# Kernel tuning notes

Hardware: AMD Instinct MI355X
Metric: run time of the kernel (lower is better)

Reference implementation:

```python
import jax, jax.numpy as jnp
import numpy as np

B, S, F = 16, 511, 128           # batch, input seq len, n_features
D, H, NB = 512, 8, 6             # embedding_dim, n_heads, n_blocks
DH = D // H                      # d_head
MLP = 4 * D                      # mlp_ratio=4 hard-coded in FxtBlock
OUT = 1                          # out_d
T = S + 1                        # tokens incl. cls
EPS = 1e-5                       # torch LayerNorm default eps


def pos_emb(seq_len, d):
    # matches get_positional_embeddings: sin for even j, cos for odd j (with j-1 exponent)
    i = np.arange(seq_len, dtype=np.float32)[:, None]
    j = np.arange(d)
    je = np.where(j % 2 == 0, j, j - 1).astype(np.float32)
    ang = i / (10000.0 ** (je / d))
    pe = np.where(j % 2 == 0, np.sin(ang), np.cos(ang))
    return jnp.asarray(pe, jnp.float32)


def layernorm(x, g, b):
    m = jnp.mean(x, axis=-1, keepdims=True)
    v = jnp.mean((x - m) ** 2, axis=-1, keepdims=True)
    return (x - m) * jax.lax.rsqrt(v + EPS) * g + b


def setup_inputs() -> dict:
    key = jax.random.key(0)
    ks = jax.random.split(key, 12)
    g = lambda k, shape: jax.random.normal(k, shape, jnp.float32) * 0.02
    return {
        "src": jax.random.normal(ks[0], (B, S, F), jnp.float32),
        "emb_W": g(ks[1], (F, D)), "emb_b": jnp.zeros((D,), jnp.float32),
        "cls_tok": jax.random.uniform(ks[2], (1, D), jnp.float32),
        "ln1_g": jnp.ones((NB, D), jnp.float32), "ln1_b": jnp.zeros((NB, D), jnp.float32),
        "Wq": g(ks[3], (NB, H, DH, DH)), "bq": jnp.zeros((NB, H, DH), jnp.float32),
        "Wk": g(ks[4], (NB, H, DH, DH)), "bk": jnp.zeros((NB, H, DH), jnp.float32),
        "Wv": g(ks[5], (NB, H, DH, DH)), "bv": jnp.zeros((NB, H, DH), jnp.float32),
        "ln2_g": jnp.ones((NB, D), jnp.float32), "ln2_b": jnp.zeros((NB, D), jnp.float32),
        "W1": g(ks[6], (NB, D, MLP)), "b1": jnp.zeros((NB, MLP), jnp.float32),
        "W2": g(ks[7], (NB, MLP, D)), "b2": jnp.zeros((NB, D), jnp.float32),
        "head_W": g(ks[8], (D, OUT)), "head_b": jnp.zeros((OUT,), jnp.float32),
    }


def reference(src, emb_W, emb_b, cls_tok, ln1_g, ln1_b, Wq, bq, Wk, bk, Wv, bv,
              ln2_g, ln2_b, W1, b1, W2, b2, head_W, head_b):
    b = src.shape[0]
    x = src @ emb_W + emb_b                                    # [B,S,D]
    cls = jnp.broadcast_to(cls_tok[None], (b, 1, D))
    x = jnp.concatenate([cls, x], axis=1) + pos_emb(T, D)[None]  # [B,T,D]
    scale = 1.0 / jnp.sqrt(jnp.float32(DH))
    for i in range(NB):
        h = layernorm(x, ln1_g[i], ln1_b[i])
        hh = h.reshape(b, T, H, DH)
        q = jnp.einsum('bthd,hde->bhte', hh, Wq[i]) + bq[i][None, :, None, :]
        k = jnp.einsum('bthd,hde->bhte', hh, Wk[i]) + bk[i][None, :, None, :]
        v = jnp.einsum('bthd,hde->bhte', hh, Wv[i]) + bv[i][None, :, None, :]
        attn = jax.nn.softmax(jnp.einsum('bhse,bhte->bhst', q, k) * scale, axis=-1)
        o = jnp.einsum('bhst,bhte->bhse', attn, v)             # [B,H,T,DH]
        x = x + o.transpose(0, 2, 1, 3).reshape(b, T, D)
        h2 = layernorm(x, ln2_g[i], ln2_b[i])
        x = x + (jax.nn.gelu(h2 @ W1[i] + b1[i], approximate=False) @ W2[i] + b2[i])
    return jax.nn.sigmoid(x[:, 0] @ head_W + head_b)           # [B,OUT]
```

## Files before the change

### kernel.cpp

```cpp
#include <hip/hip_runtime.h>
#include <hip/hip_bf16.h>
#include <math.h>

#define B 16
#define S 511
#define F 128
#define D 512
#define H 8
#define NB 6
#define DH 64
#define MLPD 2048
#define T 512
#define EPS 1e-5f

typedef unsigned short ushort;
typedef __attribute__((ext_vector_type(8))) short short8;
typedef __attribute__((ext_vector_type(4))) float floatx4;

__device__ __forceinline__ ushort f2bf(float f) {
    union { float f; unsigned u; } cv; cv.f = f;
    unsigned r = (cv.u + 0x7fff + ((cv.u >> 16) & 1)) >> 16;
    return (ushort)r;
}

__device__ __forceinline__ float fast_gelu(float x) {
    float z = fabsf(x) * 0.70710678118f;
    float t = 1.0f / (1.0f + 0.3275911f * z);
    float p = ((((1.061405429f * t - 1.453152027f) * t + 1.421413741f) * t
               - 0.284496736f) * t + 0.254829592f) * t;
    float erfv = 1.0f - p * __expf(-z * z);
    erfv = copysignf(erfv, x);
    return 0.5f * x * (1.0f + erfv);
}

__global__ void castsrc_kernel(const float* __restrict__ src, ushort* __restrict__ srcb) {
    int row = blockIdx.x;
    int t = row & (T - 1), b = row >> 9;
    int tid = threadIdx.x;
    ushort v = 0;
    if (t > 0) v = f2bf(src[((size_t)b * S + (t - 1)) * F + tid]);
    srcb[(size_t)row * F + tid] = v;
}

__global__ void wtrans_kernel(const float* __restrict__ W,
                              ushort* __restrict__ Wt,
                              int K, int N) {
    int kb = blockIdx.x * 32, nb = blockIdx.y * 32, mat = blockIdx.z;
    __shared__ float tile[32][33];
    int tid = threadIdx.x;
    int c = tid & 31, r0 = tid >> 5;
    const float* Wm = W + (size_t)mat * K * N;
    ushort* Wtm = Wt + (size_t)mat * K * N;
    #pragma unroll
    for (int l = 0; l < 4; ++l) {
        int r = r0 + l * 8;
        tile[r][c] = Wm[(size_t)(kb + r) * N + nb + c];
    }
    __syncthreads();
    #pragma unroll
    for (int l = 0; l < 4; ++l) {
        int r = r0 + l * 8;
        Wtm[(size_t)(nb + r) * K + kb + c] = f2bf(tile[c][r]);
    }
}

__global__ void wtransq_kernel(const float* __restrict__ Wq, const float* __restrict__ Wk,
                               const float* __restrict__ Wv,
                               ushort* __restrict__ WqT, ushort* __restrict__ WkT,
                               ushort* __restrict__ WvT) {
    int mat = blockIdx.x;
    int which = blockIdx.y;
    const float* W = (which == 0 ? Wq : which == 1 ? Wk : Wv) + (size_t)mat * 4096;
    ushort* O = (which == 0 ? WqT : which == 1 ? WkT : WvT) + (size_t)mat * 4096;
    __shared__ float t[64][65];
    int tid = threadIdx.x;
    int r0 = tid >> 6, c = tid & 63;
    #pragma unroll
    for (int l = 0; l < 16; ++l) {
        int row = r0 * 16 + l;
        t[row][c] = W[row * 64 + c];
    }
    __syncthreads();
    #pragma unroll
    for (int l = 0; l < 16; ++l) {
        int row = r0 * 16 + l;
        O[row * 64 + c] = f2bf(t[c][row]);
    }
}

__device__ __forceinline__ void gload_lds16(const ushort* g, ushort* l) {
    __builtin_amdgcn_global_load_lds((const __attribute__((address_space(1))) unsigned int*)g,
                                     (__attribute__((address_space(3))) unsigned int*)l,
                                     16, 0, 0);
}

#define S_WAITCNT_VM(N) asm volatile("s_waitcnt vmcnt(" #N ")" ::: "memory")

__global__ __launch_bounds__(256) void embed_gemm(const ushort* __restrict__ A,
                                                  const ushort* __restrict__ Bt,
                                                  const float* __restrict__ emb_b,
                                                  const float* __restrict__ cls_tok,
                                                  float* __restrict__ x) {
    __shared__ ushort As[64 * 32];
    __shared__ ushort Bs[64 * 32];
    int tid = threadIdx.x;
    int lane = tid & 63;
    int w = __builtin_amdgcn_readfirstlane(tid >> 6);
    int quad = lane >> 4, l15 = lane & 15;
    int wr = (w >> 1) * 32, wc = (w & 1) * 32;
    int m0 = blockIdx.x * 64, n0 = blockIdx.y * 64;

    floatx4 acc[2][2];
    #pragma unroll
    for (int i = 0; i < 2; ++i)
        #pragma unroll
        for (int j = 0; j < 2; ++j) acc[i][j] = (floatx4)0.f;

    int lrow = lane >> 2;
    int lk = (lane & 3) * 8;
    const ushort* Ag = A + (size_t)(m0 + 16 * w + lrow) * F + lk;
    const ushort* Bg = Bt + (size_t)(n0 + 16 * w + lrow) * F + lk;
    ushort* AsW = &As[16 * w * 32];
    ushort* BsW = &Bs[16 * w * 32];
    int fa = l15 * 32 + quad * 8;

    for (int kt = 0; kt < F; kt += 32) {
        gload_lds16(Ag + kt, AsW);
        gload_lds16(Bg + kt, BsW);
        __syncthreads();
        short8 af[2], bf[2];
        #pragma unroll
        for (int i = 0; i < 2; ++i) af[i] = *(const short8*)&As[(wr + 16 * i) * 32 + fa];
        #pragma unroll
        for (int j = 0; j < 2; ++j) bf[j] = *(const short8*)&Bs[(wc + 16 * j) * 32 + fa];
        #pragma unroll
        for (int i = 0; i < 2; ++i)
            #pragma unroll
            for (int j = 0; j < 2; ++j)
                acc[i][j] = __builtin_amdgcn_mfma_f32_16x16x32_bf16(af[i], bf[j], acc[i][j], 0, 0, 0);
        __syncthreads();
    }

    const float LOG1E4 = 9.210340371976184f;
    int rbase = (lane >> 4) * 4;
    int cidx = lane & 15;
    #pragma unroll
    for (int j = 0; j < 2; ++j) {
        int gc = n0 + wc + 16 * j + cidx;
        float je = (float)(gc & ~1);
        float freq = expf(-(je / (float)D) * LOG1E4);
        float ebv = emb_b[gc];
        float clsv = cls_tok[gc];
        bool odd = (gc & 1);
        #pragma unroll
        for (int i = 0; i < 2; ++i) {
            int gr = m0 + wr + 16 * i + rbase;
            #pragma unroll
            for (int reg = 0; reg < 4; ++reg) {
                int row = gr + reg;
                int t = row & (T - 1);
                float ang = (float)t * freq;
                float pe = odd ? cosf(ang) : sinf(ang);
                float val = (t == 0) ? (clsv + pe) : (acc[i][j][reg] + ebv + pe);
                x[(size_t)row * D + gc] = val;
            }
        }
    }
}

__global__ __launch_bounds__(256) void ln_kernel(const float* __restrict__ xin,
                                                 const float* __restrict__ g,
                                                 const float* __restrict__ bb,
                                                 ushort* __restrict__ out) {
    int lane = threadIdx.x & 63;
    int row = blockIdx.x * 4 + (threadIdx.x >> 6);
    const float* xr = xin + (size_t)row * D + lane * 8;
    float4 a0 = *(const float4*)xr;
    float4 a1 = *(const float4*)(xr + 4);
    float s = a0.x + a0.y + a0.z + a0.w + a1.x + a1.y + a1.z + a1.w;
    #pragma unroll
    for (int off = 1; off < 64; off <<= 1) s += __shfl_xor(s, off);
    float mean = s * (1.0f / (float)D);
    float d0 = a0.x - mean, d1 = a0.y - mean, d2 = a0.z - mean, d3 = a0.w - mean;
    float d4 = a1.x - mean, d5 = a1.y - mean, d6 = a1.z - mean, d7 = a1.w - mean;
    float sq = d0*d0 + d1*d1 + d2*d2 + d3*d3 + d4*d4 + d5*d5 + d6*d6 + d7*d7;
    #pragma unroll
    for (int off = 1; off < 64; off <<= 1) sq += __shfl_xor(sq, off);
    float rstd = rsqrtf(sq * (1.0f / (float)D) + EPS);
    const float* gp = g + lane * 8;
    const float* bp = bb + lane * 8;
    float4 g0 = *(const float4*)gp, g1 = *(const float4*)(gp + 4);
    float4 b0 = *(const float4*)bp, b1 = *(const float4*)(bp + 4);
    short8 o;
    o[0] = (short)f2bf(d0 * rstd * g0.x + b0.x);
    o[1] = (short)f2bf(d1 * rstd * g0.y + b0.y);
    o[2] = (short)f2bf(d2 * rstd * g0.z + b0.z);
    o[3] = (short)f2bf(d3 * rstd * g0.w + b0.w);
    o[4] = (short)f2bf(d4 * rstd * g1.x + b1.x);
    o[5] = (short)f2bf(d5 * rstd * g1.y + b1.y);
    o[6] = (short)f2bf(d6 * rstd * g1.z + b1.z);
    o[7] = (short)f2bf(d7 * rstd * g1.w + b1.w);
    *(short8*)(out + (size_t)row * D + lane * 8) = o;
}

__global__ __launch_bounds__(256) void ln_fuse_kernel(float* __restrict__ x,
                                                      const float* __restrict__ p0,
                                                      const float* __restrict__ g,
                                                      const float* __restrict__ bb,
                                                      ushort* __restrict__ out) {
    int lane = threadIdx.x & 63;
    int row = blockIdx.x * 4 + (threadIdx.x >> 6);
    size_t base = (size_t)row * D + lane * 8;
    float* xr = x + base;
    float4 a0 = *(const float4*)xr;
    float4 a1 = *(const float4*)(xr + 4);
    float4 q0 = *(const float4*)(p0 + base);
    float4 q1 = *(const float4*)(p0 + base + 4);
    a0.x += q0.x; a0.y += q0.y; a0.z += q0.z; a0.w += q0.w;
    a1.x += q1.x; a1.y += q1.y; a1.z += q1.z; a1.w += q1.w;
    *(float4*)xr = a0;
    *(float4*)(xr + 4) = a1;
    float s = a0.x + a0.y + a0.z + a0.w + a1.x + a1.y + a1.z + a1.w;
    #pragma unroll
    for (int off = 1; off < 64; off <<= 1) s += __shfl_xor(s, off);
    float mean = s * (1.0f / (float)D);
    float d0 = a0.x - mean, d1 = a0.y - mean, d2 = a0.z - mean, d3 = a0.w - mean;
    float d4 = a1.x - mean, d5 = a1.y - mean, d6 = a1.z - mean, d7 = a1.w - mean;
    float sq = d0*d0 + d1*d1 + d2*d2 + d3*d3 + d4*d4 + d5*d5 + d6*d6 + d7*d7;
    #pragma unroll
    for (int off = 1; off < 64; off <<= 1) sq += __shfl_xor(sq, off);
    float rstd = rsqrtf(sq * (1.0f / (float)D) + EPS);
    const float* gp = g + lane * 8;
    const float* bp = bb + lane * 8;
    float4 g0 = *(const float4*)gp, g1 = *(const float4*)(gp + 4);
    float4 b0 = *(const float4*)bp, b1 = *(const float4*)(bp + 4);
    short8 o;
    o[0] = (short)f2bf(d0 * rstd * g0.x + b0.x);
    o[1] = (short)f2bf(d1 * rstd * g0.y + b0.y);
    o[2] = (short)f2bf(d2 * rstd * g0.z + b0.z);
    o[3] = (short)f2bf(d3 * rstd * g0.w + b0.w);
    o[4] = (short)f2bf(d4 * rstd * g1.x + b1.x);
    o[5] = (short)f2bf(d5 * rstd * g1.y + b1.y);
    o[6] = (short)f2bf(d6 * rstd * g1.z + b1.z);
    o[7] = (short)f2bf(d7 * rstd * g1.w + b1.w);
    *(short8*)(out + (size_t)row * D + lane * 8) = o;
}

__global__ __launch_bounds__(256) void qkv_kernel(
        const ushort* __restrict__ hb,
        const ushort* __restrict__ WqT, const float* __restrict__ bq,
        const ushort* __restrict__ WkT, const float* __restrict__ bk,
        const ushort* __restrict__ WvT, const float* __restrict__ bv,
        ushort* __restrict__ qo, ushort* __restrict__ ko, ushort* __restrict__ vTo) {
    int m0 = blockIdx.x * 128;
    int hh = blockIdx.y;
    int tid = threadIdx.x;
    int lane = tid & 63;
    int w = __builtin_amdgcn_readfirstlane(tid >> 6);
    int quad = lane >> 4, l15 = lane & 15;

    short8 af[2][2];
    #pragma unroll
    for (int mt = 0; mt < 2; ++mt) {
        const ushort* ab = hb + (size_t)(m0 + w * 32 + mt * 16 + l15) * D + hh * DH + quad * 8;
        af[mt][0] = *(const short8*)(ab);
        af[mt][1] = *(const short8*)(ab + 32);
    }

    floatx4 acc[3][2][4];
    #pragma unroll
    for (int xo = 0; xo < 3; ++xo)
        #pragma unroll
        for (int mt = 0; mt < 2; ++mt)
            #pragma unroll
            for (int nt = 0; nt < 4; ++nt) acc[xo][mt][nt] = (floatx4)0.f;

    #pragma unroll
    for (int xo = 0; xo < 3; ++xo) {
        const ushort* WT = (xo == 0 ? WqT : xo == 1 ? WkT : WvT) + (size_t)hh * 4096;
        #pragma unroll
        for (int nt = 0; nt < 4; ++nt) {
            const ushort* wb = WT + (size_t)(nt * 16 + l15) * 64 + quad * 8;
            short8 bf0 = *(const short8*)(wb);
            short8 bf1 = *(const short8*)(wb + 32);
            #pragma unroll
            for (int mt = 0; mt < 2; ++mt) {
                acc[xo][mt][nt] = __builtin_amdgcn_mfma_f32_16x16x32_bf16(af[mt][0], bf0, acc[xo][mt][nt], 0, 0, 0);
                acc[xo][mt][nt] = __builtin_amdgcn_mfma_f32_16x16x32_bf16(af[mt][1], bf1, acc[xo][mt][nt], 0, 0, 0);
            }
        }
    }

    int bb = m0 >> 9;
    int bh = bb * H + hh;
    #pragma unroll
    for (int mt = 0; mt < 2; ++mt) {
        int trow = m0 + w * 32 + mt * 16 + quad * 4;
        int tt = trow & (T - 1);
        #pragma unroll
        for (int nt = 0; nt < 4; ++nt) {
            int col = nt * 16 + l15;
            float bqv = bq[hh * DH + col];
            float bkv = bk[hh * DH + col];
            float bvv = bv[hh * DH + col];
            #pragma unroll
            for (int reg = 0; reg < 4; ++reg) {
                qo[((size_t)bh * T + tt + reg) * DH + col] = f2bf(acc[0][mt][nt][reg] + bqv);
                ko[((size_t)bh * T + tt + reg) * DH + col] = f2bf(acc[1][mt][nt][reg] + bkv);
                vTo[((size_t)bh * DH + col) * T + tt + reg] = f2bf(acc[2][mt][nt][reg] + bvv);
            }
        }
    }
}

#define PSTRIDE 88
__global__ __launch_bounds__(256) void attn_kernel(const ushort* __restrict__ q,
                                                   const ushort* __restrict__ k,
                                                   const ushort* __restrict__ vT,
                                                   float* __restrict__ x) {
    int bh = blockIdx.x;
    int qt = blockIdx.y;
    int b = bh >> 3, hh = bh & 7;
    int tid = threadIdx.x;
    int lane = tid & 63;
    int w = __builtin_amdgcn_readfirstlane(tid >> 6);
    int quad = lane >> 4, l15 = lane & 15;

    __shared__ __align__(16) ushort smem[22016];
    ushort* Pw = smem + 16384 + w * (16 * PSTRIDE);

    const ushort* qbase = q + ((size_t)bh * T + qt * 64 + w * 16 + l15) * DH + quad * 8;
    short8 Qf0 = *(const short8*)(qbase);
    short8 Qf1 = *(const short8*)(qbase + 32);

    const ushort* kbase = k + (size_t)bh * T * DH;
    const ushort* vbase = vT + (size_t)bh * DH * T;

    int srow = lane >> 2;
    int scol = (lane & 3) * 8;
    const ushort* kg = kbase + (size_t)(w * 16 + srow) * DH + scol;
    const ushort* vg = vbase + (size_t)(w * 16 + srow) * T + scol;
    ushort* ldsK = smem + w * 16 * 32;
    ushort* ldsV = smem + 8192 + w * 16 * 32;

    float l_i[4] = {0.f, 0.f, 0.f, 0.f};
    floatx4 O[4];
    #pragma unroll
    for (int j = 0; j < 4; ++j) O[j] = (floatx4)0.f;

    gload_lds16(kg, ldsK);
    gload_lds16(kg + 32, ldsK + 2048);
    gload_lds16(vg, ldsV);
    gload_lds16(vg + 32, ldsV + 2048);
    __syncthreads();

    for (int kt = 0; kt < T / 64; ++kt) {
        int cur = kt & 1;
        if (kt < T / 64 - 1) {
            int nb = cur ^ 1;
            const ushort* kgn = kg + (size_t)(kt + 1) * 64 * DH;
            const ushort* vgn = vg + (kt + 1) * 64;
            gload_lds16(kgn, ldsK + nb * 4096);
            gload_lds16(kgn + 32, ldsK + nb * 4096 + 2048);
            gload_lds16(vgn, ldsV + nb * 4096);
            gload_lds16(vgn + 32, ldsV + nb * 4096 + 2048);
        }
        const ushort* Kc = smem + cur * 4096;
        const ushort* Vc = smem + 8192 + cur * 4096;

        floatx4 sc[4];
        #pragma unroll
        for (int j = 0; j < 4; ++j) {
            int ro = (j * 16 + l15) * 32 + quad * 8;
            short8 kf0 = *(const short8*)&Kc[ro];
            short8 kf1 = *(const short8*)&Kc[2048 + ro];
            floatx4 s4 = (floatx4)0.f;
            s4 = __builtin_amdgcn_mfma_f32_16x16x32_bf16(Qf0, kf0, s4, 0, 0, 0);
            s4 = __builtin_amdgcn_mfma_f32_16x16x32_bf16(Qf1, kf1, s4, 0, 0, 0);
            sc[j] = s4;
        }
        #pragma unroll
        for (int j = 0; j < 4; ++j) {
            #pragma unroll
            for (int r = 0; r < 4; ++r) {
                float p = __expf(sc[j][r] * 0.125f);
                ushort pb = f2bf(p);
                union { unsigned u; float f; } cv; cv.u = ((unsigned)pb) << 16;
                l_i[r] += cv.f;
                Pw[(quad * 4 + r) * PSTRIDE + j * 16 + l15] = pb;
            }
        }

        short8 af0 = *(const short8*)&Pw[l15 * PSTRIDE + quad * 8];
        short8 af1 = *(const short8*)&Pw[l15 * PSTRIDE + 32 + quad * 8];
        #pragma unroll
        for (int j = 0; j < 4; ++j) {
            int ro = (j * 16 + l15) * 32 + quad * 8;
            short8 vf0 = *(const short8*)&Vc[ro];
            short8 vf1 = *(const short8*)&Vc[2048 + ro];
            O[j] = __builtin_amdgcn_mfma_f32_16x16x32_bf16(af0, vf0, O[j], 0, 0, 0);
            O[j] = __builtin_amdgcn_mfma_f32_16x16x32_bf16(af1, vf1, O[j], 0, 0, 0);
        }
        __syncthreads();
    }

    #pragma unroll
    for (int r = 0; r < 4; ++r) {
        l_i[r] += __shfl_xor(l_i[r], 1);
        l_i[r] += __shfl_xor(l_i[r], 2);
        l_i[r] += __shfl_xor(l_i[r], 4);
        l_i[r] += __shfl_xor(l_i[r], 8);
    }

    float* Ow = (float*)smem + w * 16 * 68;
    #pragma unroll
    for (int r = 0; r < 4; ++r) {
        float rl = 1.0f / l_i[r];
        #pragma unroll
        for (int j = 0; j < 4; ++j)
            Ow[(quad * 4 + r) * 68 + j * 16 + l15] = O[j][r] * rl;
    }
    __syncthreads();
    int r4 = lane >> 4;
    int c16 = lane & 15;
    #pragma unroll
    for (int i = 0; i < 4; ++i) {
        int lrow = i * 4 + r4;
        float4 o = *(const float4*)&Ow[lrow * 68 + c16 * 4];
        int grow = qt * 64 + w * 16 + lrow;
        float* xp = &x[((size_t)(b * T) + grow) * D + hh * DH + c16 * 4];
        float4 xv = *(const float4*)xp;
        xv.x += o.x; xv.y += o.y; xv.z += o.z; xv.w += o.w;
        *(float4*)xp = xv;
    }
}

template<int EPI>
__global__ __launch_bounds__(256, 2) void gemm_db(const ushort* __restrict__ A,
                                                  const ushort* __restrict__ Bt,
                                                  const float* __restrict__ bias,
                                                  void* __restrict__ Cout,
                                                  int N, int K) {
    constexpr int BK = 64;
    __shared__ ushort lds0[256 * BK];
    __shared__ ushort lds1[256 * BK];

    int tid = threadIdx.x;
    int lane = tid & 63;
    int w = __builtin_amdgcn_readfirstlane(tid >> 6);
    int quad = lane >> 4, l15 = lane & 15;
    int wrow = (w >> 1) * 64;
    int wcol = (w & 1) * 64;

    int nwg = gridDim.x;
    int id = blockIdx.x;
    int idx = (id & 7) * (nwg >> 3) + (id >> 3);
    int NTg = N >> 7;
    int mt = idx / NTg;
    int nt = idx - mt * NTg;
    int m0 = mt * 128, n0 = nt * 128;

    int lrow = tid >> 3;
    int lslot = tid & 7;
    int scol = (lslot ^ (lrow & 7)) * 8;
    const ushort* Asrc = A + (size_t)(m0 + lrow) * K + scol;
    const ushort* Bsrc = Bt + (size_t)(n0 + lrow) * K + scol;
    int ldsAoff = (w * 8) * BK;
    int ldsBoff = 128 * BK + (w * 8) * BK;

    int sx0 = ((quad) ^ (l15 & 7)) * 8;
    int sx1 = ((4 + quad) ^ (l15 & 7)) * 8;

    floatx4 acc[4][4];
    #pragma unroll
    for (int i = 0; i < 4; ++i)
        #pragma unroll
        for (int n = 0; n < 4; ++n) acc[i][n] = (floatx4)0.f;

    #define STAGE(t, Lb) do {                                                     \
        const ushort* ap_ = Asrc + (size_t)(t) * BK;                              \
        const ushort* bp_ = Bsrc + (size_t)(t) * BK;                              \
        _Pragma("unroll")                                                         \
        for (int j = 0; j < 4; ++j)                                               \
            gload_lds16(ap_ + (size_t)j * 32 * K, (Lb) + ldsAoff + j * 32 * BK);  \
        _Pragma("unroll")                                                         \
        for (int j = 0; j < 4; ++j)                                               \
            gload_lds16(bp_ + (size_t)j * 32 * K, (Lb) + ldsBoff + j * 32 * BK);  \
    } while (0)

    #define COMP(Lb) do {                                                         \
        const ushort* Ab_ = (Lb);                                                 \
        const ushort* Bb_ = (Lb) + 128 * BK;                                      \
        _Pragma("unroll")                                                         \
        for (int ks = 0; ks < 2; ++ks) {                                          \
            int sx_ = ks ? sx1 : sx0;                                             \
            short8 bfr[4];                                                        \
            _Pragma("unroll")                                                     \
            for (int n = 0; n < 4; ++n)                                           \
                bfr[n] = *(const short8*)&Bb_[(wcol + n * 16 + l15) * BK + sx_];  \
            _Pragma("unroll")                                                     \
            for (int i = 0; i < 4; ++i) {                                         \
                short8 af_ = *(const short8*)&Ab_[(wrow + i * 16 + l15) * BK + sx_]; \
                _Pragma("unroll")                                                 \
                for (int n = 0; n < 4; ++n)                                       \
                    acc[i][n] = __builtin_amdgcn_mfma_f32_16x16x32_bf16(af_, bfr[n], acc[i][n], 0, 0, 0); \
            }                                                                     \
        }                                                                         \
    } while (0)

    int NT = K >> 6;
    STAGE(0, lds0);
    for (int t = 0; t < NT - 2; t += 2) {
        STAGE(t + 1, lds1);
        S_WAITCNT_VM(8);
        __builtin_amdgcn_s_barrier();
        __builtin_amdgcn_s_setprio(1);
        COMP(lds0);
        __builtin_amdgcn_s_setprio(0);
        asm volatile("s_waitcnt lgkmcnt(0)" ::: "memory");
        __builtin_amdgcn_s_barrier();
        STAGE(t + 2, lds0);
        S_WAITCNT_VM(8);
        __builtin_amdgcn_s_barrier();
        __builtin_amdgcn_s_setprio(1);
        COMP(lds1);
        __builtin_amdgcn_s_setprio(0);
        asm volatile("s_waitcnt lgkmcnt(0)" ::: "memory");
        __builtin_amdgcn_s_barrier();
    }
    STAGE(NT - 1, lds1);
    S_WAITCNT_VM(8);
    __builtin_amdgcn_s_barrier();
    __builtin_amdgcn_s_setprio(1);
    COMP(lds0);
    __builtin_amdgcn_s_setprio(0);
    asm volatile("s_waitcnt lgkmcnt(0)" ::: "memory");
    __builtin_amdgcn_s_barrier();
    S_WAITCNT_VM(0);
    __builtin_amdgcn_s_barrier();
    COMP(lds1);

    #undef STAGE
    #undef COMP

    int rbase = quad * 4;
    #pragma unroll
    for (int i = 0; i < 4; ++i) {
        #pragma unroll
        for (int n = 0; n < 4; ++n) {
            int gc = n0 + wcol + n * 16 + l15;
            float bv = bias[gc];
            int gr = m0 + wrow + i * 16 + rbase;
            #pragma unroll
            for (int reg = 0; reg < 4; ++reg) {
                if constexpr (EPI == 0) {
                    ((ushort*)Cout)[(size_t)(gr + reg) * N + gc] =
                        f2bf(fast_gelu(acc[i][n][reg] + bv));
                } else {
                    ((float*)Cout)[(size_t)(gr + reg) * N + gc] = acc[i][n][reg] + bv;
                }
            }
        }
    }
}

__global__ void head_kernel(const float* __restrict__ x,
                            const float* __restrict__ p0,
                            const float* __restrict__ hw,
                            const float* __restrict__ hb,
                            float* __restrict__ out) {
    int b = blockIdx.x;
    int tid = threadIdx.x;
    size_t idx = (size_t)b * T * D + tid;
    float s = (x[idx] + p0[idx]) * hw[tid];
    #pragma unroll
    for (int off = 32; off > 0; off >>= 1) s += __shfl_down(s, off, 64);
    __shared__ float red[8];
    if ((tid & 63) == 0) red[tid >> 6] = s;
    __syncthreads();
    if (tid == 0) {
        float t = 0.f;
        #pragma unroll
        for (int i = 0; i < 8; ++i) t += red[i];
        out[b] = 1.0f / (1.0f + __expf(-(t + hb[0])));
    }
}

extern "C" void kernel_launch(void* const* d_in, const int* in_sizes, int n_in,
                              void* d_out, int out_size, void* d_ws, size_t ws_size,
                              hipStream_t stream) {
    const float* src     = (const float*)d_in[0];
    const float* emb_W   = (const float*)d_in[1];
    const float* emb_b   = (const float*)d_in[2];
    const float* cls_tok = (const float*)d_in[3];
    const float* ln1_g   = (const float*)d_in[4];
    const float* ln1_b   = (const float*)d_in[5];
    const float* Wq      = (const float*)d_in[6];
    const float* bq      = (const float*)d_in[7];
    const float* Wk      = (const float*)d_in[8];
    const float* bk      = (const float*)d_in[9];
    const float* Wv      = (const float*)d_in[10];
    const float* bv      = (const float*)d_in[11];
    const float* ln2_g   = (const float*)d_in[12];
    const float* ln2_b   = (const float*)d_in[13];
    const float* W1      = (const float*)d_in[14];
    const float* b1      = (const float*)d_in[15];
    const float* W2      = (const float*)d_in[16];
    const float* b2      = (const float*)d_in[17];
    const float* head_W  = (const float*)d_in[18];
    const float* head_b  = (const float*)d_in[19];

    const size_t NTOK = (size_t)B * T;
    char* wsb = (char*)d_ws;
    float*  x    = (float*)wsb;      wsb += NTOK * D * 4;
    float*  p0   = (float*)wsb;      wsb += NTOK * D * 4;
    ushort* hbuf = (ushort*)wsb;     wsb += NTOK * D * 2;
    ushort* q    = (ushort*)wsb;     wsb += NTOK * D * 2;
    ushort* k    = (ushort*)wsb;     wsb += NTOK * D * 2;
    ushort* vT   = (ushort*)wsb;     wsb += NTOK * D * 2;
    ushort* u    = (ushort*)wsb;     wsb += NTOK * MLPD * 2;
    ushort* W1t  = (ushort*)wsb;     wsb += (size_t)NB * D * MLPD * 2;
    ushort* W2t  = (ushort*)wsb;     wsb += (size_t)NB * D * MLPD * 2;
    ushort* WqT  = (ushort*)wsb;     wsb += (size_t)NB * H * DH * DH * 2;
    ushort* WkT  = (ushort*)wsb;     wsb += (size_t)NB * H * DH * DH * 2;
    ushort* WvT  = (ushort*)wsb;     wsb += (size_t)NB * H * DH * DH * 2;
    ushort* srcb = (ushort*)wsb;     wsb += NTOK * F * 2;
    ushort* embWt= (ushort*)wsb;     wsb += (size_t)F * D * 2;

    wtrans_kernel<<<dim3(D / 32, MLPD / 32, NB), 256, 0, stream>>>(W1, W1t, D, MLPD);
    wtrans_kernel<<<dim3(MLPD / 32, D / 32, NB), 256, 0, stream>>>(W2, W2t, MLPD, D);
    wtransq_kernel<<<dim3(NB * H, 3), 256, 0, stream>>>(Wq, Wk, Wv, WqT, WkT, WvT);
    wtrans_kernel<<<dim3(F / 32, D / 32, 1), 256, 0, stream>>>(emb_W, embWt, F, D);
    castsrc_kernel<<<B * T, F, 0, stream>>>(src, srcb);

    embed_gemm<<<dim3(B * T / 64, D / 64), 256, 0, stream>>>(srcb, embWt, emb_b, cls_tok, x);

    for (int i = 0; i < NB; ++i) {
        if (i == 0)
            ln_kernel<<<B * T / 4, 256, 0, stream>>>(x, ln1_g, ln1_b, hbuf);
        else
            ln_fuse_kernel<<<B * T / 4, 256, 0, stream>>>(x, p0,
                ln1_g + i * D, ln1_b + i * D, hbuf);
        qkv_kernel<<<dim3(B * T / 128, H), 256, 0, stream>>>(hbuf,
            WqT + (size_t)i * H * DH * DH, bq + (size_t)i * H * DH,
            WkT + (size_t)i * H * DH * DH, bk + (size_t)i * H * DH,
            WvT + (size_t)i * H * DH * DH, bv + (size_t)i * H * DH,
            q, k, vT);
        attn_kernel<<<dim3(B * H, T / 64), 256, 0, stream>>>(q, k, vT, x);
        ln_kernel<<<B * T / 4, 256, 0, stream>>>(x, ln2_g + i * D, ln2_b + i * D, hbuf);
        gemm_db<0><<<dim3((B * T / 128) * (MLPD / 128)), 256, 0, stream>>>(
            hbuf, W1t + (size_t)i * D * MLPD, b1 + (size_t)i * MLPD, u, MLPD, D);
        gemm_db<1><<<dim3((B * T / 128) * (D / 128)), 256, 0, stream>>>(
            u, W2t + (size_t)i * MLPD * D, b2 + (size_t)i * D, p0, D, MLPD);
    }

    head_kernel<<<B, 512, 0, stream>>>(x, p0, head_W, head_b, (float*)d_out);
}
```

Measured before the change: 848.9 us.

## Add 256x256-tile 8-wave GEMM with phased load/MFMA interleave for MLP up-projection

```diff
diff --git a/kernel.cpp b/kernel.cpp
--- a/kernel.cpp
+++ b/kernel.cpp
@@ -95,6 +95,7 @@
 }
 
 #define S_WAITCNT_VM(N) asm volatile("s_waitcnt vmcnt(" #N ")" ::: "memory")
+#define S_WAITCNT_LGKM0 asm volatile("s_waitcnt lgkmcnt(0)" ::: "memory")
 
 __global__ __launch_bounds__(256) void embed_gemm(const ushort* __restrict__ A,
                                                   const ushort* __restrict__ Bt,
@@ -435,11 +436,151 @@
     }
 }
 
-template<int EPI>
+__global__ __launch_bounds__(512, 2) void gemm1_8ph(const ushort* __restrict__ A,
+                                                    const ushort* __restrict__ Bt,
+                                                    const float* __restrict__ bias,
+                                                    ushort* __restrict__ C,
+                                                    int N, int K) {
+    constexpr int BK = 64;
+    constexpr int BUF = 32768;
+    constexpr int BOF = 16384;
+    __shared__ ushort lds[2 * BUF];
+
+    int tid = threadIdx.x;
+    int lane = tid & 63;
+    int w = __builtin_amdgcn_readfirstlane(tid >> 6);
+    int quad = lane >> 4, l15 = lane & 15;
+    int wm = w >> 2, wn = w & 3;
+    int wmr = wm * 128, wnr = wn * 64;
+
+    int nwg = gridDim.x;
+    int id = blockIdx.x;
+    int idx = (id & 7) * (nwg >> 3) + (id >> 3);
+    int NTg = N >> 8;
+    int mt = idx / NTg, nt = idx - mt * NTg;
+    int m0 = mt * 256, n0 = nt * 256;
+
+    int rr = tid >> 3;
+    int scol = ((tid & 7) ^ (rr & 7)) * 8;
+    const ushort* AgS = A + (size_t)(m0 + rr) * K + scol;
+    const ushort* BgS = Bt + (size_t)(n0 + rr) * K + scol;
+    int woff = (w * 8) * BK;
+
+    int sx0 = (quad ^ (l15 & 7)) * 8;
+    int sx1 = ((4 + quad) ^ (l15 & 7)) * 8;
+
+    floatx4 acc[8][4];
+    #pragma unroll
+    for (int i = 0; i < 8; ++i)
+        #pragma unroll
+        for (int n = 0; n < 4; ++n) acc[i][n] = (floatx4)0.f;
+
+    short8 a[4][2], b[4][2];
+
+    #define STG_A(th, h, bb) do {                                                          \
+        gload_lds16(AgS + (size_t)((h) * 128) * K + (size_t)(th) * BK,                     \
+                    (bb) + ((h) * 128) * BK + woff);                                       \
+        gload_lds16(AgS + (size_t)((h) * 128 + 64) * K + (size_t)(th) * BK,                \
+                    (bb) + ((h) * 128 + 64) * BK + woff);                                  \
+    } while (0)
+    #define STG_B(th, h, bb) do {                                                          \
+        gload_lds16(BgS + (size_t)((h) * 128) * K + (size_t)(th) * BK,                     \
+                    (bb) + BOF + ((h) * 128) * BK + woff);                                 \
+        gload_lds16(BgS + (size_t)((h) * 128 + 64) * K + (size_t)(th) * BK,                \
+                    (bb) + BOF + ((h) * 128 + 64) * BK + woff);                            \
+    } while (0)
+
+    #define MFMA_Q(mb, nb2) do {                                                           \
+        _Pragma("unroll")                                                                  \
+        for (int ks = 0; ks < 2; ++ks)                                                     \
+            _Pragma("unroll")                                                              \
+            for (int i = 0; i < 4; ++i)                                                    \
+                _Pragma("unroll")                                                          \
+                for (int n = 0; n < 2; ++n)                                                \
+                    acc[(mb) + i][(nb2) + n] = __builtin_amdgcn_mfma_f32_16x16x32_bf16(    \
+                        a[i][ks], b[(nb2) + n][ks], acc[(mb) + i][(nb2) + n], 0, 0, 0);    \
+    } while (0)
+
+    STG_A(0, 0, lds); STG_A(0, 1, lds); STG_B(0, 0, lds); STG_B(0, 1, lds);
+    STG_A(1, 0, lds + BUF);
+
+    int NT = K >> 6;
+    for (int t = 0; t < NT; ++t) {
+        ushort* bufc = lds + (t & 1) * BUF;
+        ushort* bufn = lds + (((t & 1) ^ 1)) * BUF;
+        bool sn = (t + 1 < NT);
+        if (t == NT - 1) { S_WAITCNT_VM(0); } else { S_WAITCNT_VM(2); }
+        __builtin_amdgcn_s_barrier();
+        #pragma unroll
+        for (int ks = 0; ks < 2; ++ks) {
+            int sx = ks ? sx1 : sx0;
+            #pragma unroll
+            for (int i = 0; i < 4; ++i)
+                a[i][ks] = *(const short8*)&bufc[(wmr + i * 16 + l15) * BK + sx];
+            #pragma unroll
+            for (int n = 0; n < 2; ++n)
+                b[n][ks] = *(const short8*)&bufc[BOF + (wnr + n * 16 + l15) * BK + sx];
+        }
+        if (sn) STG_A(t + 1, 1, bufn);
+        S_WAITCNT_LGKM0;
+        __builtin_amdgcn_s_setprio(1);
+        MFMA_Q(0, 0);
+        __builtin_amdgcn_s_setprio(0);
+        #pragma unroll
+        for (int ks = 0; ks < 2; ++ks) {
+            int sx = ks ? sx1 : sx0;
+            #pragma unroll
+            for (int n = 0; n < 2; ++n)
+                b[2 + n][ks] = *(const short8*)&bufc[BOF + (wnr + (2 + n) * 16 + l15) * BK + sx];
+        }
+        if (sn) STG_B(t + 1, 0, bufn);
+        S_WAITCNT_LGKM0;
+        __builtin_amdgcn_s_setprio(1);
+        MFMA_Q(0, 2);
+        __builtin_amdgcn_s_setprio(0);
+        #pragma unroll
+        for (int ks = 0; ks < 2; ++ks) {
+            int sx = ks ? sx1 : sx0;
+            #pragma unroll
+            for (int i = 0; i < 4; ++i)
+                a[i][ks] = *(const short8*)&bufc[(wmr + (4 + i) * 16 + l15) * BK + sx];
+        }
+        if (sn) STG_B(t + 1, 1, bufn);
+        S_WAITCNT_LGKM0;
+        __builtin_amdgcn_s_setprio(1);
+        MFMA_Q(4, 2);
+        __builtin_amdgcn_s_setprio(0);
+        __builtin_amdgcn_s_barrier();
+        if (t + 2 < NT) STG_A(t + 2, 0, bufc);
+        __builtin_amdgcn_s_setprio(1);
+        MFMA_Q(4, 0);
+        __builtin_amdgcn_s_setprio(0);
+    }
+
+    #undef STG_A
+    #undef STG_B
+    #undef MFMA_Q
+
+    int rbase = quad * 4;
+    #pragma unroll
+    for (int i = 0; i < 8; ++i) {
+        #pragma unroll
+        for (int n = 0; n < 4; ++n) {
+            int gc = n0 + wnr + n * 16 + l15;
+            float bv = bias[gc];
+            int gr = m0 + wmr + i * 16 + rbase;
+            #pragma unroll
+            for (int reg = 0; reg < 4; ++reg) {
+                C[(size_t)(gr + reg) * N + gc] = f2bf(fast_gelu(acc[i][n][reg] + bv));
+            }
+        }
+    }
+}
+
 __global__ __launch_bounds__(256, 2) void gemm_db(const ushort* __restrict__ A,
                                                   const ushort* __restrict__ Bt,
                                                   const float* __restrict__ bias,
-                                                  void* __restrict__ Cout,
+                                                  float* __restrict__ Cout,
                                                   int N, int K) {
     constexpr int BK = 64;
     __shared__ ushort lds0[256 * BK];
@@ -517,7 +658,7 @@
         __builtin_amdgcn_s_setprio(1);
         COMP(lds0);
         __builtin_amdgcn_s_setprio(0);
-        asm volatile("s_waitcnt lgkmcnt(0)" ::: "memory");
+        S_WAITCNT_LGKM0;
         __builtin_amdgcn_s_barrier();
         STAGE(t + 2, lds0);
         S_WAITCNT_VM(8);
@@ -525,7 +666,7 @@
         __builtin_amdgcn_s_setprio(1);
         COMP(lds1);
         __builtin_amdgcn_s_setprio(0);
-        asm volatile("s_waitcnt lgkmcnt(0)" ::: "memory");
+        S_WAITCNT_LGKM0;
         __builtin_amdgcn_s_barrier();
     }
     STAGE(NT - 1, lds1);
@@ -534,7 +675,7 @@
     __builtin_amdgcn_s_setprio(1);
     COMP(lds0);
     __builtin_amdgcn_s_setprio(0);
-    asm volatile("s_waitcnt lgkmcnt(0)" ::: "memory");
+    S_WAITCNT_LGKM0;
     __builtin_amdgcn_s_barrier();
     S_WAITCNT_VM(0);
     __builtin_amdgcn_s_barrier();
@@ -553,12 +694,7 @@
             int gr = m0 + wrow + i * 16 + rbase;
             #pragma unroll
             for (int reg = 0; reg < 4; ++reg) {
-                if constexpr (EPI == 0) {
-                    ((ushort*)Cout)[(size_t)(gr + reg) * N + gc] =
-                        f2bf(fast_gelu(acc[i][n][reg] + bv));
-                } else {
-                    ((float*)Cout)[(size_t)(gr + reg) * N + gc] = acc[i][n][reg] + bv;
-                }
+                Cout[(size_t)(gr + reg) * N + gc] = acc[i][n][reg] + bv;
             }
         }
     }
@@ -648,9 +784,9 @@
             q, k, vT);
         attn_kernel<<<dim3(B * H, T / 64), 256, 0, stream>>>(q, k, vT, x);
         ln_kernel<<<B * T / 4, 256, 0, stream>>>(x, ln2_g + i * D, ln2_b + i * D, hbuf);
-        gemm_db<0><<<dim3((B * T / 128) * (MLPD / 128)), 256, 0, stream>>>(
+        gemm1_8ph<<<dim3((B * T / 256) * (MLPD / 256)), 512, 0, stream>>>(
             hbuf, W1t + (size_t)i * D * MLPD, b1 + (size_t)i * MLPD, u, MLPD, D);
-        gemm_db<1><<<dim3((B * T / 128) * (D / 128)), 256, 0, stream>>>(
+        gemm_db<<<dim3((B * T / 128) * (D / 128)), 256, 0, stream>>>(
             u, W2t + (size_t)i * MLPD * D, b2 + (size_t)i * D, p0, D, MLPD);
     }
 
```

New measurement: 837.6 us. Within noise of the previous version (-1.3%).
